# Optimization experiments

Measured on AMD Instinct MI355X. Metric: run time of the kernel, lower is better.

The kernel has to match this reference:

```python
import jax, jax.numpy as jnp
import numpy as np

DIM = 1024
HEADS = 16
HEAD_DIM = DIM // HEADS


def setup_inputs() -> dict:
    key = jax.random.key(0)
    ks = jax.random.split(key, 7)
    scale = 1.0 / np.sqrt(DIM)
    x = jax.random.normal(ks[0], (2, 2048, DIM), dtype=jnp.float32)
    Wq = jax.random.uniform(ks[1], (DIM, DIM), jnp.float32, -scale, scale)
    bq = jax.random.uniform(ks[2], (DIM,), jnp.float32, -scale, scale)
    Wk = jax.random.uniform(ks[3], (DIM, DIM), jnp.float32, -scale, scale)
    bk = jax.random.uniform(ks[4], (DIM,), jnp.float32, -scale, scale)
    Wv = jax.random.uniform(ks[5], (DIM, DIM), jnp.float32, -scale, scale)
    bv = jax.random.uniform(ks[6], (DIM,), jnp.float32, -scale, scale)
    return {"x": x, "Wq": Wq, "bq": bq, "Wk": Wk, "bk": bk, "Wv": Wv, "bv": bv}


def reference(x, Wq, bq, Wk, bk, Wv, bv):
    b, s, _ = x.shape
    # torch Linear: y = x @ W.T + b
    q = (x @ Wq.T + bq).reshape(b, s, HEADS, HEAD_DIM)
    k = (x @ Wk.T + bk).reshape(b, s, HEADS, HEAD_DIM)
    v = (x @ Wv.T + bv).reshape(b, s, HEADS, HEAD_DIM)
    # scores: (b, s, z, h), softmax over z (key axis = axis 2)
    scores = jnp.einsum('bshd,bzhd->bszh', q, k) / jnp.sqrt(jnp.float32(HEAD_DIM))
    attention = jax.nn.softmax(scores, axis=2)
    output = jnp.einsum('bzhd,bszh->bshd', v, attention)
    return output
```

## Files before the change

### kernel.cpp

```cpp
#include <hip/hip_runtime.h>
#include <hip/hip_bf16.h>

typedef unsigned short u16;
typedef __attribute__((ext_vector_type(8))) __bf16 bf16x8;
typedef __attribute__((ext_vector_type(4))) float f32x4;
typedef __attribute__((ext_vector_type(8))) u16 u16x8;

#define BATCH 2
#define SEQ   2048
#define DIM   1024
#define HEADS 16
#define HDIM  64

#define QSCALE 0.18033688011112042f

__device__ __forceinline__ float bf2f(u16 u) {
  union { unsigned int u; float f; } v; v.u = ((unsigned int)u) << 16; return v.f;
}
__device__ __forceinline__ u16 f2bf(float f) {
  union { float f; unsigned int u; } v; v.f = f;
  unsigned int r = v.u + 0x7fffu + ((v.u >> 16) & 1u);
  return (u16)(r >> 16);
}
__device__ __forceinline__ unsigned int pk2(float a, float b) {
  union { __hip_bfloat162 h2; unsigned int u; } v;
  v.h2 = __float22bfloat162_rn(float2{a, b});
  return v.u;
}

__device__ __forceinline__ void async16(u16* lds, const u16* g) {
  __builtin_amdgcn_global_load_lds(
      (__attribute__((address_space(1))) void*)(void*)(g),
      (__attribute__((address_space(3))) void*)(lds), 16, 0, 0);
}

#define XG  524288
#define WG  131072
extern "C" __global__ __launch_bounds__(256)
void convert_all(const float* __restrict__ x,  const float* __restrict__ wq,
                 const float* __restrict__ wk, const float* __restrict__ wv,
                 u16* __restrict__ xbf, u16* __restrict__ wbf)
{
  const int g = blockIdx.x * 256 + threadIdx.x;
  const float* src; u16* dst; size_t off;
  if (g < XG)               { src = x;  dst = xbf;                 off = (size_t)g; }
  else if (g < XG + WG)     { src = wq; dst = wbf;                 off = (size_t)(g - XG); }
  else if (g < XG + 2 * WG) { src = wk; dst = wbf + DIM * DIM;     off = (size_t)(g - XG - WG); }
  else                      { src = wv; dst = wbf + 2 * DIM * DIM; off = (size_t)(g - XG - 2 * WG); }
  f32x4 a = *(const f32x4*)(src + off * 8);
  f32x4 b = *(const f32x4*)(src + off * 8 + 4);
  u16x8 o;
#pragma unroll
  for (int i = 0; i < 4; ++i) { o[i] = f2bf(a[i]); o[4 + i] = f2bf(b[i]); }
  *(u16x8*)(dst + off * 8) = o;
}

extern "C" __global__ __launch_bounds__(256)
void qkv_gemm(const u16* __restrict__ xbf, const u16* __restrict__ wbf,
              const float* __restrict__ bq, const float* __restrict__ bk,
              const float* __restrict__ bv,
              u16* __restrict__ qo, u16* __restrict__ ko, u16* __restrict__ vto)
{
  __shared__ alignas(16) u16 Albs[2][128 * 32];
  __shared__ alignas(16) u16 Blbs[2][128 * 32];

  const int which = blockIdx.z;
  const u16* Wb = wbf + (size_t)which * DIM * DIM;
  const float* bias = (which == 0) ? bq : (which == 1) ? bk : bv;

  const int lane = threadIdx.x & 63;
  const int wave = threadIdx.x >> 6;
  const int l16  = lane & 15;
  const int quad = lane >> 4;
  const int lrow = lane >> 2;
  const int lcol = (lane & 3) * 8;

  const int mBase = blockIdx.y * 128;
  const int nBase = blockIdx.x * 128;
  const int mw = (wave >> 1) * 64;
  const int nw = (wave & 1) * 64;

  f32x4 acc[4][4] = {};

#pragma unroll
  for (int p = 0; p < 2; ++p) {
    const int r16 = wave * 2 + p;
    const int row = r16 * 16 + lrow;
    async16(&Albs[0][r16 * 512], xbf + (size_t)(mBase + row) * DIM + lcol);
    async16(&Blbs[0][r16 * 512], Wb  + (size_t)(nBase + row) * DIM + lcol);
  }

  for (int it = 0; it < 32; ++it) {
    const int bb = it & 1;
    if (it < 31) {
      __syncthreads();
      const int k0n = (it + 1) * 32;
#pragma unroll
      for (int p = 0; p < 2; ++p) {
        const int r16 = wave * 2 + p;
        const int row = r16 * 16 + lrow;
        async16(&Albs[bb ^ 1][r16 * 512], xbf + (size_t)(mBase + row) * DIM + k0n + lcol);
        async16(&Blbs[bb ^ 1][r16 * 512], Wb  + (size_t)(nBase + row) * DIM + k0n + lcol);
      }
      asm volatile("s_waitcnt vmcnt(4)" ::: "memory");
    } else {
      asm volatile("s_waitcnt vmcnt(0)" ::: "memory");
    }
    __syncthreads();

    bf16x8 af[4], bfr[4];
#pragma unroll
    for (int i = 0; i < 4; ++i) {
      af[i]  = *(const bf16x8*)&Albs[bb][(mw + i * 16 + l16) * 32 + quad * 8];
      bfr[i] = *(const bf16x8*)&Blbs[bb][(nw + i * 16 + l16) * 32 + quad * 8];
    }
#pragma unroll
    for (int mi = 0; mi < 4; ++mi)
#pragma unroll
      for (int ni = 0; ni < 4; ++ni)
        acc[mi][ni] = __builtin_amdgcn_mfma_f32_16x16x32_bf16(af[mi], bfr[ni], acc[mi][ni], 0, 0, 0);
  }

  const float oscale = (which == 0) ? QSCALE : 1.0f;
#pragma unroll
  for (int ni = 0; ni < 4; ++ni) {
    const int n = nBase + nw + ni * 16 + l16;
    const float bval = bias[n];
    const int h = n >> 6, d = n & 63;
#pragma unroll
    for (int mi = 0; mi < 4; ++mi) {
#pragma unroll
      for (int r = 0; r < 4; ++r) {
        const int m = mBase + mw + mi * 16 + quad * 4 + r;
        const int bi = m >> 11, s = m & 2047;
        const u16 val = f2bf((acc[mi][ni][r] + bval) * oscale);
        if (which == 2) {
          vto[((size_t)(bi * HEADS + h) * HDIM + d) * SEQ + s] = val;
        } else {
          u16* dst = (which == 0) ? qo : ko;
          dst[((size_t)(bi * HEADS + h) * SEQ + s) * HDIM + d] = val;
        }
      }
    }
  }
}

extern "C" __global__ __launch_bounds__(256)
void attn(const u16* __restrict__ q, const u16* __restrict__ k,
          const u16* __restrict__ vt, float* __restrict__ out)
{
  __shared__ alignas(16) u16 Klds[2][64 * 64];
  __shared__ alignas(16) u16 Vlds[2][64 * 64];
  __shared__ alignas(16) u16 Plds[4][32 * 64];

  const int lane = threadIdx.x & 63;
  const int wave = threadIdx.x >> 6;
  const int l16  = lane & 15;
  const int quad = lane >> 4;
  const int r8   = lane >> 3;
  const int sl   = lane & 7;
  const int jsw  = sl ^ (r8 & 7);
  const int e7   = l16 & 7;

  const int h     = blockIdx.y;
  const int b     = blockIdx.z;
  const int qbase = blockIdx.x * 128 + wave * 32;

  const u16* qh  = q  + (size_t)(b * HEADS + h) * SEQ * HDIM;
  const u16* kh  = k  + (size_t)(b * HEADS + h) * SEQ * HDIM;
  const u16* vth = vt + (size_t)(b * HEADS + h) * HDIM * SEQ;

  bf16x8 qf[2][2];
#pragma unroll
  for (int qg = 0; qg < 2; ++qg)
#pragma unroll
    for (int ks = 0; ks < 2; ++ks)
      qf[qg][ks] = *(const bf16x8*)(qh + (size_t)(qbase + qg * 16 + l16) * HDIM + ks * 32 + quad * 8);

  float lsum[2] = {};
  f32x4 o[2][4] = {};
  u16* pw = &Plds[wave][0];

#pragma unroll
  for (int p = 0; p < 2; ++p) {
    const int i = wave * 2 + p;
    async16(&Klds[0][i * 512], kh  + (size_t)(i * 8 + r8) * HDIM + jsw * 8);
    async16(&Vlds[0][i * 512], vth + (size_t)(i * 8 + r8) * SEQ + jsw * 8);
  }

  for (int it = 0; it < 32; ++it) {
    const int bb = it & 1;
    if (it < 31) {
      __syncthreads();
      const int kb1 = (it + 1) * 64;
#pragma unroll
      for (int p = 0; p < 2; ++p) {
        const int i = wave * 2 + p;
        async16(&Klds[bb ^ 1][i * 512], kh  + (size_t)(kb1 + i * 8 + r8) * HDIM + jsw * 8);
        async16(&Vlds[bb ^ 1][i * 512], vth + (size_t)(i * 8 + r8) * SEQ + kb1 + jsw * 8);
      }
      asm volatile("s_waitcnt vmcnt(4)" ::: "memory");
    } else {
      asm volatile("s_waitcnt vmcnt(0)" ::: "memory");
    }
    __syncthreads();

    const u16* Kb = &Klds[bb][0];
    const u16* Vb = &Vlds[bb][0];

    f32x4 sc[2][4] = {};
#pragma unroll
    for (int ks = 0; ks < 2; ++ks) {
#pragma unroll
      for (int nt = 0; nt < 4; ++nt) {
        bf16x8 kf = *(const bf16x8*)&Kb[(nt * 16 + l16) * 64 + ((ks * 4 + quad) ^ e7) * 8];
#pragma unroll
        for (int qg = 0; qg < 2; ++qg)
          sc[qg][nt] = __builtin_amdgcn_mfma_f32_16x16x32_bf16(kf, qf[qg][ks], sc[qg][nt], 0, 0, 0);
      }
    }

#pragma unroll
    for (int qg = 0; qg < 2; ++qg) {
      float ls = 0.f;
#pragma unroll
      for (int nt = 0; nt < 4; ++nt) {
        const float p0 = __builtin_exp2f(sc[qg][nt][0]);
        const float p1 = __builtin_exp2f(sc[qg][nt][1]);
        const float p2 = __builtin_exp2f(sc[qg][nt][2]);
        const float p3 = __builtin_exp2f(sc[qg][nt][3]);
        ls += (p0 + p1) + (p2 + p3);
        uint2 pkv; pkv.x = pk2(p0, p1); pkv.y = pk2(p2, p3);
        *(uint2*)(pw + (qg * 16 + l16) * 64
                  + ((nt * 2 + (quad >> 1)) ^ e7) * 8 + (quad & 1) * 4) = pkv;
      }
      lsum[qg] += ls;
    }

#pragma unroll
    for (int ks = 0; ks < 2; ++ks) {
      bf16x8 pf0 = *(const bf16x8*)&pw[(0 * 16 + l16) * 64 + ((ks * 4 + quad) ^ e7) * 8];
      bf16x8 pf1 = *(const bf16x8*)&pw[(1 * 16 + l16) * 64 + ((ks * 4 + quad) ^ e7) * 8];
#pragma unroll
      for (int dt = 0; dt < 4; ++dt) {
        bf16x8 vfr = *(const bf16x8*)&Vb[(dt * 16 + l16) * 64 + ((ks * 4 + quad) ^ e7) * 8];
        o[0][dt] = __builtin_amdgcn_mfma_f32_16x16x32_bf16(pf0, vfr, o[0][dt], 0, 0, 0);
        o[1][dt] = __builtin_amdgcn_mfma_f32_16x16x32_bf16(pf1, vfr, o[1][dt], 0, 0, 0);
      }
    }
  }

#pragma unroll
  for (int qg = 0; qg < 2; ++qg) {
    lsum[qg] += __shfl_xor(lsum[qg], 16, 64);
    lsum[qg] += __shfl_xor(lsum[qg], 32, 64);
  }
  asm volatile("s_waitcnt lgkmcnt(0)" ::: "memory");
  float* lw = (float*)pw;
  if (lane < 16) { lw[lane] = lsum[0]; lw[16 + lane] = lsum[1]; }
  asm volatile("s_waitcnt lgkmcnt(0)" ::: "memory");

#pragma unroll
  for (int qg = 0; qg < 2; ++qg) {
#pragma unroll
    for (int r = 0; r < 4; ++r) {
      const float inv = 1.f / fmaxf(lw[qg * 16 + quad * 4 + r], 1e-20f);
      const int s = qbase + qg * 16 + quad * 4 + r;
#pragma unroll
      for (int dt = 0; dt < 4; ++dt) {
        const int d = dt * 16 + l16;
        out[((size_t)(b * SEQ + s) * HEADS + h) * HDIM + d] = o[qg][dt][r] * inv;
      }
    }
  }
}

extern "C" void kernel_launch(void* const* d_in, const int* in_sizes, int n_in,
                              void* d_out, int out_size, void* d_ws, size_t ws_size,
                              hipStream_t stream) {
  (void)in_sizes; (void)n_in; (void)out_size; (void)ws_size;
  const float* x  = (const float*)d_in[0];
  const float* Wq = (const float*)d_in[1];
  const float* bq = (const float*)d_in[2];
  const float* Wk = (const float*)d_in[3];
  const float* bk = (const float*)d_in[4];
  const float* Wv = (const float*)d_in[5];
  const float* bv = (const float*)d_in[6];
  float* out = (float*)d_out;

  u16* ws = (u16*)d_ws;
  const size_t XSZ = (size_t)BATCH * SEQ * DIM;
  const size_t WSZ = (size_t)DIM * DIM;
  const size_t QSZ = (size_t)BATCH * HEADS * SEQ * HDIM;
  u16* xbf   = ws;
  u16* wbf   = ws + XSZ;
  u16* qbuf  = ws + XSZ + 3 * WSZ;
  u16* kbuf  = qbuf + QSZ;
  u16* vtbuf = kbuf + QSZ;

  convert_all<<<3584, 256, 0, stream>>>(x, Wq, Wk, Wv, xbf, wbf);

  dim3 g1(DIM / 128, (BATCH * SEQ) / 128, 3);
  qkv_gemm<<<g1, 256, 0, stream>>>(xbf, wbf, bq, bk, bv, qbuf, kbuf, vtbuf);

  dim3 g2(SEQ / 128, HEADS, BATCH);
  attn<<<g2, 256, 0, stream>>>(qbuf, kbuf, vtbuf, out);
}
```

Before: 200.0 us.

## Triple-buffer attention K/V with software-pipelined QK^T and swizzle GEMM LDS

The attention kernel moves to a three-stage K/V ring buffer and issues the QK^T MFMAs for the next tile while the current tile's softmax and PV work is in flight. It also changes the P tile LDS swizzle to 4-element granularity. The QKV GEMM drops its double buffering in favor of a single 64-wide K tile with an XOR-swizzled LDS layout, which halves the number of iterations but waits for loads at vmcnt(0) on every step. The trade-offs are more LDS per attention block, which could lower occupancy, and lost load/compute overlap in the GEMM.

```diff
diff --git a/kernel.cpp b/kernel.cpp
--- a/kernel.cpp
+++ b/kernel.cpp
@@ -61,8 +61,8 @@
               const float* __restrict__ bv,
               u16* __restrict__ qo, u16* __restrict__ ko, u16* __restrict__ vto)
 {
-  __shared__ alignas(16) u16 Albs[2][128 * 32];
-  __shared__ alignas(16) u16 Blbs[2][128 * 32];
+  __shared__ alignas(16) u16 Albs[128 * 64];
+  __shared__ alignas(16) u16 Blbs[128 * 64];
 
   const int which = blockIdx.z;
   const u16* Wb = wbf + (size_t)which * DIM * DIM;
@@ -72,8 +72,10 @@
   const int wave = threadIdx.x >> 6;
   const int l16  = lane & 15;
   const int quad = lane >> 4;
-  const int lrow = lane >> 2;
-  const int lcol = (lane & 3) * 8;
+  const int r8   = lane >> 3;
+  const int sl   = lane & 7;
+  const int jsw  = sl ^ (r8 & 7);
+  const int e7   = l16 & 7;
 
   const int mBase = blockIdx.y * 128;
   const int nBase = blockIdx.x * 128;
@@ -82,43 +84,32 @@
 
   f32x4 acc[4][4] = {};
 
-#pragma unroll
-  for (int p = 0; p < 2; ++p) {
-    const int r16 = wave * 2 + p;
-    const int row = r16 * 16 + lrow;
-    async16(&Albs[0][r16 * 512], xbf + (size_t)(mBase + row) * DIM + lcol);
-    async16(&Blbs[0][r16 * 512], Wb  + (size_t)(nBase + row) * DIM + lcol);
-  }
-
-  for (int it = 0; it < 32; ++it) {
-    const int bb = it & 1;
-    if (it < 31) {
-      __syncthreads();
-      const int k0n = (it + 1) * 32;
-#pragma unroll
-      for (int p = 0; p < 2; ++p) {
-        const int r16 = wave * 2 + p;
-        const int row = r16 * 16 + lrow;
-        async16(&Albs[bb ^ 1][r16 * 512], xbf + (size_t)(mBase + row) * DIM + k0n + lcol);
-        async16(&Blbs[bb ^ 1][r16 * 512], Wb  + (size_t)(nBase + row) * DIM + k0n + lcol);
-      }
-      asm volatile("s_waitcnt vmcnt(4)" ::: "memory");
-    } else {
-      asm volatile("s_waitcnt vmcnt(0)" ::: "memory");
-    }
+  for (int k0 = 0; k0 < DIM; k0 += 64) {
+#pragma unroll
+    for (int p = 0; p < 4; ++p) {
+      const int i = wave * 4 + p;
+      async16(&Albs[i * 512], xbf + (size_t)(mBase + i * 8 + r8) * DIM + k0 + jsw * 8);
+      async16(&Blbs[i * 512], Wb  + (size_t)(nBase + i * 8 + r8) * DIM + k0 + jsw * 8);
+    }
+    asm volatile("s_waitcnt vmcnt(0)" ::: "memory");
     __syncthreads();
 
-    bf16x8 af[4], bfr[4];
-#pragma unroll
-    for (int i = 0; i < 4; ++i) {
-      af[i]  = *(const bf16x8*)&Albs[bb][(mw + i * 16 + l16) * 32 + quad * 8];
-      bfr[i] = *(const bf16x8*)&Blbs[bb][(nw + i * 16 + l16) * 32 + quad * 8];
-    }
-#pragma unroll
-    for (int mi = 0; mi < 4; ++mi)
-#pragma unroll
-      for (int ni = 0; ni < 4; ++ni)
-        acc[mi][ni] = __builtin_amdgcn_mfma_f32_16x16x32_bf16(af[mi], bfr[ni], acc[mi][ni], 0, 0, 0);
+    bf16x8 af[4][2], bfr[4][2];
+#pragma unroll
+    for (int i = 0; i < 4; ++i)
+#pragma unroll
+      for (int ks = 0; ks < 2; ++ks) {
+        af[i][ks]  = *(const bf16x8*)&Albs[(mw + i * 16 + l16) * 64 + ((ks * 4 + quad) ^ e7) * 8];
+        bfr[i][ks] = *(const bf16x8*)&Blbs[(nw + i * 16 + l16) * 64 + ((ks * 4 + quad) ^ e7) * 8];
+      }
+#pragma unroll
+    for (int ks = 0; ks < 2; ++ks)
+#pragma unroll
+      for (int mi = 0; mi < 4; ++mi)
+#pragma unroll
+        for (int ni = 0; ni < 4; ++ni)
+          acc[mi][ni] = __builtin_amdgcn_mfma_f32_16x16x32_bf16(af[mi][ks], bfr[ni][ks], acc[mi][ni], 0, 0, 0);
+    __syncthreads();
   }
 
   const float oscale = (which == 0) ? QSCALE : 1.0f;
@@ -149,8 +140,8 @@
 void attn(const u16* __restrict__ q, const u16* __restrict__ k,
           const u16* __restrict__ vt, float* __restrict__ out)
 {
-  __shared__ alignas(16) u16 Klds[2][64 * 64];
-  __shared__ alignas(16) u16 Vlds[2][64 * 64];
+  __shared__ alignas(16) u16 Klds[3][64 * 64];
+  __shared__ alignas(16) u16 Vlds[3][64 * 64];
   __shared__ alignas(16) u16 Plds[4][32 * 64];
 
   const int lane = threadIdx.x & 63;
@@ -161,6 +152,7 @@
   const int sl   = lane & 7;
   const int jsw  = sl ^ (r8 & 7);
   const int e7   = l16 & 7;
+  const int psw  = e7 * 2;
 
   const int h     = blockIdx.y;
   const int b     = blockIdx.z;
@@ -179,46 +171,42 @@
 
   float lsum[2] = {};
   f32x4 o[2][4] = {};
+  f32x4 sc[2][4] = {};
   u16* pw = &Plds[wave][0];
 
-#pragma unroll
-  for (int p = 0; p < 2; ++p) {
-    const int i = wave * 2 + p;
-    async16(&Klds[0][i * 512], kh  + (size_t)(i * 8 + r8) * HDIM + jsw * 8);
-    async16(&Vlds[0][i * 512], vth + (size_t)(i * 8 + r8) * SEQ + jsw * 8);
-  }
-
-  for (int it = 0; it < 32; ++it) {
-    const int bb = it & 1;
-    if (it < 31) {
-      __syncthreads();
-      const int kb1 = (it + 1) * 64;
-#pragma unroll
-      for (int p = 0; p < 2; ++p) {
-        const int i = wave * 2 + p;
-        async16(&Klds[bb ^ 1][i * 512], kh  + (size_t)(kb1 + i * 8 + r8) * HDIM + jsw * 8);
-        async16(&Vlds[bb ^ 1][i * 512], vth + (size_t)(i * 8 + r8) * SEQ + kb1 + jsw * 8);
-      }
-      asm volatile("s_waitcnt vmcnt(4)" ::: "memory");
-    } else {
-      asm volatile("s_waitcnt vmcnt(0)" ::: "memory");
-    }
-    __syncthreads();
-
-    const u16* Kb = &Klds[bb][0];
-    const u16* Vb = &Vlds[bb][0];
-
-    f32x4 sc[2][4] = {};
-#pragma unroll
-    for (int ks = 0; ks < 2; ++ks) {
+  auto stage = [&](int bidx, int kb) {
+#pragma unroll
+    for (int p = 0; p < 2; ++p) {
+      const int i = wave * 2 + p;
+      async16(&Klds[bidx][i * 512], kh  + (size_t)(kb + i * 8 + r8) * HDIM + jsw * 8);
+      async16(&Vlds[bidx][i * 512], vth + (size_t)(i * 8 + r8) * SEQ + kb + jsw * 8);
+    }
+  };
+  auto qkt = [&](int bidx) {
+#pragma unroll
+    for (int qg = 0; qg < 2; ++qg)
+#pragma unroll
+      for (int nt = 0; nt < 4; ++nt) sc[qg][nt] = f32x4{0.f, 0.f, 0.f, 0.f};
+#pragma unroll
+    for (int ks = 0; ks < 2; ++ks)
 #pragma unroll
       for (int nt = 0; nt < 4; ++nt) {
-        bf16x8 kf = *(const bf16x8*)&Kb[(nt * 16 + l16) * 64 + ((ks * 4 + quad) ^ e7) * 8];
+        bf16x8 kf = *(const bf16x8*)&Klds[bidx][(nt * 16 + l16) * 64 + ((ks * 4 + quad) ^ e7) * 8];
 #pragma unroll
         for (int qg = 0; qg < 2; ++qg)
           sc[qg][nt] = __builtin_amdgcn_mfma_f32_16x16x32_bf16(kf, qf[qg][ks], sc[qg][nt], 0, 0, 0);
       }
-    }
+  };
+
+  stage(0, 0);
+  stage(1, 64);
+  asm volatile("s_waitcnt vmcnt(0)" ::: "memory");
+  __syncthreads();
+  qkt(0);
+
+  int i0 = 0, i1 = 1, i2 = 2;
+  for (int t = 0; t < 32; ++t) {
+    if (t < 30) stage(i2, (t + 2) * 64);
 
 #pragma unroll
     for (int qg = 0; qg < 2; ++qg) {
@@ -231,23 +219,30 @@
         const float p3 = __builtin_exp2f(sc[qg][nt][3]);
         ls += (p0 + p1) + (p2 + p3);
         uint2 pkv; pkv.x = pk2(p0, p1); pkv.y = pk2(p2, p3);
-        *(uint2*)(pw + (qg * 16 + l16) * 64
-                  + ((nt * 2 + (quad >> 1)) ^ e7) * 8 + (quad & 1) * 4) = pkv;
+        *(uint2*)(pw + (qg * 16 + l16) * 64 + ((nt * 4 + quad) ^ psw) * 4) = pkv;
       }
       lsum[qg] += ls;
     }
 
+    if (t < 31) qkt(i1);
+
 #pragma unroll
     for (int ks = 0; ks < 2; ++ks) {
-      bf16x8 pf0 = *(const bf16x8*)&pw[(0 * 16 + l16) * 64 + ((ks * 4 + quad) ^ e7) * 8];
-      bf16x8 pf1 = *(const bf16x8*)&pw[(1 * 16 + l16) * 64 + ((ks * 4 + quad) ^ e7) * 8];
+      bf16x8 pf0 = *(const bf16x8*)&pw[(0 * 16 + l16) * 64 + ((ks * 8 + quad * 2) ^ psw) * 4];
+      bf16x8 pf1 = *(const bf16x8*)&pw[(1 * 16 + l16) * 64 + ((ks * 8 + quad * 2) ^ psw) * 4];
 #pragma unroll
       for (int dt = 0; dt < 4; ++dt) {
-        bf16x8 vfr = *(const bf16x8*)&Vb[(dt * 16 + l16) * 64 + ((ks * 4 + quad) ^ e7) * 8];
+        bf16x8 vfr = *(const bf16x8*)&Vlds[i0][(dt * 16 + l16) * 64 + ((ks * 4 + quad) ^ e7) * 8];
         o[0][dt] = __builtin_amdgcn_mfma_f32_16x16x32_bf16(pf0, vfr, o[0][dt], 0, 0, 0);
         o[1][dt] = __builtin_amdgcn_mfma_f32_16x16x32_bf16(pf1, vfr, o[1][dt], 0, 0, 0);
       }
     }
+
+    if (t < 31) {
+      asm volatile("s_waitcnt vmcnt(0)" ::: "memory");
+      __syncthreads();
+    }
+    const int tmp = i0; i0 = i1; i1 = i2; i2 = tmp;
   }
 
 #pragma unroll
```

After: 213.3 us. 1.07x slower.
